# Performance work log

Measured on AMD Instinct MI355X. Metric: run time of the kernel, lower is better.

The kernel has to match this reference:

```python
import jax, jax.numpy as jnp
import numpy as np

N_NODES = 40000
N_EDGES = 640000
D = 128
D_OUT = 128


def _layernorm(x, gamma, beta, eps=1e-5):
    mu = jnp.mean(x, axis=-1, keepdims=True)
    var = jnp.mean(jnp.square(x - mu), axis=-1, keepdims=True)
    return (x - mu) * jax.lax.rsqrt(var + eps) * gamma + beta


def setup_inputs() -> dict:
    key = jax.random.key(0)
    ks = jax.random.split(key, 6)
    x = jax.random.normal(ks[0], (N_NODES, D), dtype=jnp.float32)
    edge_index = jax.random.randint(ks[1], (2, N_EDGES), 0, N_NODES, dtype=jnp.int64)
    s = 1.0 / np.sqrt(D)
    return {
        "x": x,
        "edge_index": edge_index,
        "ln1_w": jnp.ones((D,), jnp.float32),
        "ln1_b": jnp.zeros((D,), jnp.float32),
        "ln2_w": jnp.ones((D,), jnp.float32),
        "ln2_b": jnp.zeros((D,), jnp.float32),
        "w": jnp.ones((D,), jnp.float32),
        "W1": jax.random.normal(ks[2], (D, D), jnp.float32) * s,
        "W2": jax.random.normal(ks[3], (D, D), jnp.float32) * s,
        "O1": jax.random.normal(ks[4], (2 * D, D), jnp.float32) * s,
        "O2": jax.random.normal(ks[5], (D, D_OUT), jnp.float32) * s,
    }


def reference(x, edge_index, ln1_w, ln1_b, ln2_w, ln2_b, w, W1, W2, O1, O2):
    row, col = edge_index[0], edge_index[1]
    n = x.shape[0]
    # gather + 2-layer message MLP (bias-free): [E, D]
    msg = jnp.maximum(x[row] @ W1, 0.0) @ W2
    # scatter_mean over destination nodes (zero where no incoming edges)
    agg = jax.ops.segment_sum(msg, col, num_segments=n)
    cnt = jax.ops.segment_sum(jnp.ones((msg.shape[0],), x.dtype), col, num_segments=n)
    agg = agg / jnp.maximum(cnt, 1.0)[:, None]
    agg_n = _layernorm(agg, ln1_w, ln1_b)
    # repulsion + residual + LayerNorm
    fx = _layernorm(x + (x - agg_n) * w, ln2_w, ln2_b)
    # concat + output MLP
    cat = jnp.concatenate([fx, agg_n], axis=1)
    return jnp.maximum(cat @ O1, 0.0) @ O2
```

## Files before the change

kernel.cpp:

```cpp
#include <hip/hip_runtime.h>
#include <hip/hip_bf16.h>

#define NN 40000
#define NE 640000
#define DD 128
#define CAP 64

typedef __attribute__((ext_vector_type(8))) short bf16x8;
typedef __attribute__((ext_vector_type(8))) unsigned short u16x8;
typedef __attribute__((ext_vector_type(4))) float f32x4;

__device__ __forceinline__ unsigned short f2bf(float f) {
    __hip_bfloat16 h = __float2bfloat16(f);
    return *reinterpret_cast<unsigned short*>(&h);
}
__device__ __forceinline__ float bf2f(unsigned short u) {
    union { unsigned int ui; float f; } v;
    v.ui = ((unsigned int)u) << 16;
    return v.f;
}
__device__ __forceinline__ void gload16(void* lds, const void* g) {
    __builtin_amdgcn_global_load_lds(
        (const __attribute__((address_space(1))) void*)g,
        (__attribute__((address_space(3))) void*)lds, 16, 0, 0);
}

__global__ __launch_bounds__(256) void prep_kernel(
    const float* __restrict__ W1, const float* __restrict__ W2,
    const float* __restrict__ O1, const float* __restrict__ O2,
    unsigned short* __restrict__ w1t, unsigned short* __restrict__ w2t,
    unsigned short* __restrict__ o1t, unsigned short* __restrict__ o2t,
    unsigned int* __restrict__ cnt)
{
    int bx = blockIdx.x;
    if (bx >= 320) {
        int t = (bx - 320) * 256 + threadIdx.x;
        if (t < NN) cnt[t * 16] = 0u;
        return;
    }
    int t = bx * 256 + threadIdx.x;
    if (t < 16384) {
        int n = t >> 7, k = t & 127;
        unsigned b = (unsigned)(n * 256) + (((unsigned)(k * 2)) ^ (((unsigned)(n & 7)) << 4));
        w1t[b >> 1] = f2bf(W1[k * 128 + n]);
    } else if (t < 32768) {
        int i = t - 16384;
        int n = i >> 7, k = i & 127;
        unsigned b = (unsigned)(n * 256) + (((unsigned)(k * 2)) ^ (((unsigned)(n & 7)) << 4));
        w2t[b >> 1] = f2bf(W2[k * 128 + n]);
    } else if (t < 65536) {
        int i = t - 32768;
        int n = i >> 8, k = i & 255;
        unsigned b = (unsigned)(n * 512 + (k >> 7) * 256)
                   + (((unsigned)((k & 127) * 2)) ^ (((unsigned)(n & 7)) << 4));
        o1t[b >> 1] = f2bf(O1[k * 128 + n]);
    } else {
        int i = t - 65536;
        int n = i >> 7, k = i & 127;
        unsigned b = (unsigned)(n * 256) + (((unsigned)(k * 2)) ^ (((unsigned)(n & 7)) << 4));
        o2t[b >> 1] = f2bf(O2[k * 128 + n]);
    }
}

__global__ __launch_bounds__(256) void mlp1_kernel(
    const float* __restrict__ x, const unsigned short* __restrict__ w1t,
    const unsigned short* __restrict__ w2t, unsigned short* __restrict__ nm)
{
    __shared__ unsigned short xt[64 * 128];
    __shared__ unsigned short wb[128 * 128];
    const int tid = threadIdx.x;
    const int row0 = blockIdx.x * 64;
    const int lane = tid & 63;
    const int wv = tid >> 6;

    #pragma unroll
    for (int it = 0; it < 8; ++it) {
        int b = (wv * 8 + it) * 1024;
        gload16((char*)wb + b, (const char*)w1t + b + lane * 16);
    }
    #pragma unroll
    for (int it = 0; it < 4; ++it) {
        int c = tid + it * 256;
        int r = c >> 4;
        int c0 = (c & 15) << 3;
        const float4* gp = reinterpret_cast<const float4*>(x + (size_t)(row0 + r) * DD + c0);
        float4 f0 = gp[0], f1 = gp[1];
        u16x8 p;
        p[0] = f2bf(f0.x); p[1] = f2bf(f0.y); p[2] = f2bf(f0.z); p[3] = f2bf(f0.w);
        p[4] = f2bf(f1.x); p[5] = f2bf(f1.y); p[6] = f2bf(f1.z); p[7] = f2bf(f1.w);
        unsigned b = (unsigned)((r * DD + c0) * 2) ^ ((unsigned)(r & 7) << 4);
        *reinterpret_cast<u16x8*>(reinterpret_cast<char*>(xt) + b) = p;
    }
    __syncthreads();

    const int l15 = lane & 15;
    const int lg = lane >> 4;

    f32x4 acc[8];
    #pragma unroll
    for (int i = 0; i < 8; ++i) acc[i] = (f32x4){0.f, 0.f, 0.f, 0.f};

    #pragma unroll
    for (int kk = 0; kk < 4; ++kk) {
        int k = kk * 32 + lg * 8;
        int ar = wv * 16 + l15;
        bf16x8 a = *reinterpret_cast<const bf16x8*>(
            reinterpret_cast<const char*>(xt) + ((unsigned)((ar * DD + k) * 2) ^ ((unsigned)(ar & 7) << 4)));
        #pragma unroll
        for (int n0 = 0; n0 < 8; ++n0) {
            int bn = n0 * 16 + l15;
            bf16x8 bf = *reinterpret_cast<const bf16x8*>(
                reinterpret_cast<const char*>(wb) + ((unsigned)((bn * DD + k) * 2) ^ ((unsigned)(bn & 7) << 4)));
            acc[n0] = __builtin_amdgcn_mfma_f32_16x16x32_bf16(a, bf, acc[n0], 0, 0, 0);
        }
    }
    __syncthreads();

    #pragma unroll
    for (int it = 0; it < 8; ++it) {
        int b = (wv * 8 + it) * 1024;
        gload16((char*)wb + b, (const char*)w2t + b + lane * 16);
    }
    unsigned short* hb = xt;
    #pragma unroll
    for (int n0 = 0; n0 < 8; ++n0) {
        #pragma unroll
        for (int ri = 0; ri < 4; ++ri) {
            int r = wv * 16 + lg * 4 + ri;
            int cc = n0 * 16 + l15;
            float v = fmaxf(acc[n0][ri], 0.0f);
            *reinterpret_cast<unsigned short*>(
                reinterpret_cast<char*>(hb) + ((unsigned)((r * DD + cc) * 2) ^ ((unsigned)(r & 7) << 4))) = f2bf(v);
        }
    }
    __syncthreads();

    f32x4 acc2[8];
    #pragma unroll
    for (int i = 0; i < 8; ++i) acc2[i] = (f32x4){0.f, 0.f, 0.f, 0.f};
    #pragma unroll
    for (int kk = 0; kk < 4; ++kk) {
        int k = kk * 32 + lg * 8;
        int ar = wv * 16 + l15;
        bf16x8 a = *reinterpret_cast<const bf16x8*>(
            reinterpret_cast<const char*>(hb) + ((unsigned)((ar * DD + k) * 2) ^ ((unsigned)(ar & 7) << 4)));
        #pragma unroll
        for (int n0 = 0; n0 < 8; ++n0) {
            int bn = n0 * 16 + l15;
            bf16x8 bf = *reinterpret_cast<const bf16x8*>(
                reinterpret_cast<const char*>(wb) + ((unsigned)((bn * DD + k) * 2) ^ ((unsigned)(bn & 7) << 4)));
            acc2[n0] = __builtin_amdgcn_mfma_f32_16x16x32_bf16(a, bf, acc2[n0], 0, 0, 0);
        }
    }
    #pragma unroll
    for (int n0 = 0; n0 < 8; ++n0) {
        #pragma unroll
        for (int ri = 0; ri < 4; ++ri) {
            int r = row0 + wv * 16 + lg * 4 + ri;
            int cc = n0 * 16 + l15;
            nm[(size_t)r * DD + cc] = f2bf(acc2[n0][ri]);
        }
    }
}

__global__ __launch_bounds__(256) void fill_kernel(
    const int* __restrict__ ei, unsigned int* __restrict__ cnt,
    unsigned short* __restrict__ srcs)
{
    const int t = blockIdx.x * 256 + threadIdx.x;
    int s[4], d[4];
    #pragma unroll
    for (int j = 0; j < 4; ++j) d[j] = ei[NE + t + j * 160000];
    #pragma unroll
    for (int j = 0; j < 4; ++j) s[j] = ei[t + j * 160000];
    unsigned int p[4];
    #pragma unroll
    for (int j = 0; j < 4; ++j) p[j] = atomicAdd(cnt + d[j] * 16, 1u);
    #pragma unroll
    for (int j = 0; j < 4; ++j)
        if (p[j] < CAP) srcs[(size_t)d[j] * CAP + p[j]] = (unsigned short)s[j];
}

__global__ __launch_bounds__(256) void pull_node_kernel(
    const unsigned short* __restrict__ nm, const unsigned short* __restrict__ srcs,
    const unsigned int* __restrict__ cnt,
    const float* __restrict__ x,
    const float* __restrict__ g1, const float* __restrict__ b1,
    const float* __restrict__ g2, const float* __restrict__ b2,
    const float* __restrict__ w, unsigned short* __restrict__ catb)
{
    const int lane = threadIdx.x & 63;
    const int wv = threadIdx.x >> 6;
    const int i = blockIdx.x * 4 + wv;
    const int d0 = lane * 2;

    const unsigned int degf = cnt[i * 16];
    const int deg = (int)(degf < CAP ? degf : CAP);
    const unsigned short* sp = srcs + (size_t)i * CAP;

    float a0 = 0.f, a1 = 0.f;
    int e = 0;
    for (; e + 8 <= deg; e += 8) {
        int s[8];
        #pragma unroll
        for (int j = 0; j < 8; ++j) s[j] = sp[e + j];
        ushort2 m[8];
        #pragma unroll
        for (int j = 0; j < 8; ++j)
            m[j] = *reinterpret_cast<const ushort2*>(nm + (size_t)s[j] * DD + d0);
        #pragma unroll
        for (int j = 0; j < 8; ++j) { a0 += bf2f(m[j].x); a1 += bf2f(m[j].y); }
    }
    for (; e + 4 <= deg; e += 4) {
        int s0 = sp[e + 0], s1 = sp[e + 1], s2 = sp[e + 2], s3 = sp[e + 3];
        ushort2 m0 = *reinterpret_cast<const ushort2*>(nm + (size_t)s0 * DD + d0);
        ushort2 m1 = *reinterpret_cast<const ushort2*>(nm + (size_t)s1 * DD + d0);
        ushort2 m2 = *reinterpret_cast<const ushort2*>(nm + (size_t)s2 * DD + d0);
        ushort2 m3 = *reinterpret_cast<const ushort2*>(nm + (size_t)s3 * DD + d0);
        a0 += bf2f(m0.x) + bf2f(m1.x) + bf2f(m2.x) + bf2f(m3.x);
        a1 += bf2f(m0.y) + bf2f(m1.y) + bf2f(m2.y) + bf2f(m3.y);
    }
    for (; e < deg; ++e) {
        int s0 = sp[e];
        ushort2 m0 = *reinterpret_cast<const ushort2*>(nm + (size_t)s0 * DD + d0);
        a0 += bf2f(m0.x);
        a1 += bf2f(m0.y);
    }

    float inv = 1.0f / fmaxf((float)degf, 1.0f);
    a0 *= inv; a1 *= inv;

    float s = a0 + a1;
    #pragma unroll
    for (int o = 32; o > 0; o >>= 1) s += __shfl_xor(s, o, 64);
    float mu = s * (1.0f / 128.0f);
    float e0 = a0 - mu, e1 = a1 - mu;
    float q = e0 * e0 + e1 * e1;
    #pragma unroll
    for (int o = 32; o > 0; o >>= 1) q += __shfl_xor(q, o, 64);
    float rs = rsqrtf(q * (1.0f / 128.0f) + 1e-5f);

    float2 g1v = *reinterpret_cast<const float2*>(g1 + d0);
    float2 b1v = *reinterpret_cast<const float2*>(b1 + d0);
    float an0 = e0 * rs * g1v.x + b1v.x;
    float an1 = e1 * rs * g1v.y + b1v.y;

    float2 xv = *reinterpret_cast<const float2*>(x + (size_t)i * DD + d0);
    float2 wv2 = *reinterpret_cast<const float2*>(w + d0);
    float t0 = xv.x + (xv.x - an0) * wv2.x;
    float t1 = xv.y + (xv.y - an1) * wv2.y;

    float s2 = t0 + t1;
    #pragma unroll
    for (int o = 32; o > 0; o >>= 1) s2 += __shfl_xor(s2, o, 64);
    float mu2 = s2 * (1.0f / 128.0f);
    float f0 = t0 - mu2, f1 = t1 - mu2;
    float q2 = f0 * f0 + f1 * f1;
    #pragma unroll
    for (int o = 32; o > 0; o >>= 1) q2 += __shfl_xor(q2, o, 64);
    float rs2 = rsqrtf(q2 * (1.0f / 128.0f) + 1e-5f);

    float2 g2v = *reinterpret_cast<const float2*>(g2 + d0);
    float2 b2v = *reinterpret_cast<const float2*>(b2 + d0);
    float fx0 = f0 * rs2 * g2v.x + b2v.x;
    float fx1 = f1 * rs2 * g2v.y + b2v.y;

    ushort2 uo; uo.x = f2bf(fx0); uo.y = f2bf(fx1);
    *reinterpret_cast<ushort2*>(catb + (size_t)i * 256 + d0) = uo;
    ushort2 ua; ua.x = f2bf(an0); ua.y = f2bf(an1);
    *reinterpret_cast<ushort2*>(catb + (size_t)i * 256 + 128 + d0) = ua;
}

__global__ __launch_bounds__(256) void mlp2_kernel(
    const unsigned short* __restrict__ catb, const unsigned short* __restrict__ o1t,
    const unsigned short* __restrict__ o2t, float* __restrict__ out)
{
    __shared__ unsigned short ct[64 * 128];
    __shared__ unsigned short wb[128 * 128];
    const int tid = threadIdx.x;
    const int row0 = blockIdx.x * 64;
    const int lane = tid & 63;
    const int wv = tid >> 6;
    const int l15 = lane & 15;
    const int lg = lane >> 4;

    f32x4 acc[8];
    #pragma unroll
    for (int i = 0; i < 8; ++i) acc[i] = (f32x4){0.f, 0.f, 0.f, 0.f};

    for (int h = 0; h < 2; ++h) {
        #pragma unroll
        for (int it = 0; it < 8; ++it) {
            int Lb = (wv * 8 + it) * 1024;
            int n = (Lb >> 8) + (lane >> 4);
            int c2 = (lane & 15) * 16;
            gload16((char*)wb + Lb, (const char*)o1t + n * 512 + h * 256 + c2);
        }
        #pragma unroll
        for (int it = 0; it < 4; ++it) {
            int c = tid + it * 256;
            int r = c >> 4;
            int c0 = (c & 15) << 3;
            u16x8 v = *reinterpret_cast<const u16x8*>(catb + (size_t)(row0 + r) * 256 + h * 128 + c0);
            unsigned b = (unsigned)((r * 128 + c0) * 2) ^ ((unsigned)(r & 7) << 4);
            *reinterpret_cast<u16x8*>(reinterpret_cast<char*>(ct) + b) = v;
        }
        __syncthreads();
        #pragma unroll
        for (int kk = 0; kk < 4; ++kk) {
            int k = kk * 32 + lg * 8;
            int ar = wv * 16 + l15;
            bf16x8 a = *reinterpret_cast<const bf16x8*>(
                reinterpret_cast<const char*>(ct) + ((unsigned)((ar * 128 + k) * 2) ^ ((unsigned)(ar & 7) << 4)));
            #pragma unroll
            for (int n0 = 0; n0 < 8; ++n0) {
                int bn = n0 * 16 + l15;
                bf16x8 bf = *reinterpret_cast<const bf16x8*>(
                    reinterpret_cast<const char*>(wb) + ((unsigned)((bn * 128 + k) * 2) ^ ((unsigned)(bn & 7) << 4)));
                acc[n0] = __builtin_amdgcn_mfma_f32_16x16x32_bf16(a, bf, acc[n0], 0, 0, 0);
            }
        }
        __syncthreads();
    }

    #pragma unroll
    for (int it = 0; it < 8; ++it) {
        int b = (wv * 8 + it) * 1024;
        gload16((char*)wb + b, (const char*)o2t + b + lane * 16);
    }
    unsigned short* hb = ct;
    #pragma unroll
    for (int n0 = 0; n0 < 8; ++n0) {
        #pragma unroll
        for (int ri = 0; ri < 4; ++ri) {
            int r = wv * 16 + lg * 4 + ri;
            int cc = n0 * 16 + l15;
            float v = fmaxf(acc[n0][ri], 0.0f);
            *reinterpret_cast<unsigned short*>(
                reinterpret_cast<char*>(hb) + ((unsigned)((r * DD + cc) * 2) ^ ((unsigned)(r & 7) << 4))) = f2bf(v);
        }
    }
    __syncthreads();

    f32x4 acc2[8];
    #pragma unroll
    for (int i = 0; i < 8; ++i) acc2[i] = (f32x4){0.f, 0.f, 0.f, 0.f};
    #pragma unroll
    for (int kk = 0; kk < 4; ++kk) {
        int k = kk * 32 + lg * 8;
        int ar = wv * 16 + l15;
        bf16x8 a = *reinterpret_cast<const bf16x8*>(
            reinterpret_cast<const char*>(hb) + ((unsigned)((ar * DD + k) * 2) ^ ((unsigned)(ar & 7) << 4)));
        #pragma unroll
        for (int n0 = 0; n0 < 8; ++n0) {
            int bn = n0 * 16 + l15;
            bf16x8 bf = *reinterpret_cast<const bf16x8*>(
                reinterpret_cast<const char*>(wb) + ((unsigned)((bn * DD + k) * 2) ^ ((unsigned)(bn & 7) << 4)));
            acc2[n0] = __builtin_amdgcn_mfma_f32_16x16x32_bf16(a, bf, acc2[n0], 0, 0, 0);
        }
    }

    #pragma unroll
    for (int n0 = 0; n0 < 8; ++n0) {
        #pragma unroll
        for (int ri = 0; ri < 4; ++ri) {
            int r = row0 + wv * 16 + lg * 4 + ri;
            int cc = n0 * 16 + l15;
            out[(size_t)r * DD + cc] = acc2[n0][ri];
        }
    }
}

extern "C" void kernel_launch(void* const* d_in, const int* in_sizes, int n_in,
                              void* d_out, int out_size, void* d_ws, size_t ws_size,
                              hipStream_t stream) {
    const float* x   = (const float*)d_in[0];
    const int*   ei  = (const int*)d_in[1];
    const float* g1  = (const float*)d_in[2];
    const float* b1  = (const float*)d_in[3];
    const float* g2  = (const float*)d_in[4];
    const float* b2  = (const float*)d_in[5];
    const float* w   = (const float*)d_in[6];
    const float* W1  = (const float*)d_in[7];
    const float* W2  = (const float*)d_in[8];
    const float* O1  = (const float*)d_in[9];
    const float* O2  = (const float*)d_in[10];
    float* out = (float*)d_out;

    char* ws = (char*)d_ws;
    unsigned short* nm   = (unsigned short*)(ws);
    unsigned short* catb = (unsigned short*)(ws + 10240000);
    unsigned short* srcs = (unsigned short*)(ws + 30720000);
    unsigned int*   cnt  = (unsigned int*)(ws + 35840000);
    unsigned short* w1t  = (unsigned short*)(ws + 38400000);
    unsigned short* w2t  = (unsigned short*)(ws + 38432768);
    unsigned short* o1t  = (unsigned short*)(ws + 38465536);
    unsigned short* o2t  = (unsigned short*)(ws + 38531072);

    prep_kernel<<<477, 256, 0, stream>>>(W1, W2, O1, O2, w1t, w2t, o1t, o2t, cnt);
    fill_kernel<<<625, 256, 0, stream>>>(ei, cnt, srcs);
    mlp1_kernel<<<625, 256, 0, stream>>>(x, w1t, w2t, nm);
    pull_node_kernel<<<NN / 4, 256, 0, stream>>>(nm, srcs, cnt, x, g1, b1, g2, b2, w, catb);
    mlp2_kernel<<<NN / 64, 256, 0, stream>>>(catb, o1t, o2t, out);
}
```

Measured before the change: 170.1 us.

## Fuse neighbor pull and layernorms into output MLP kernel via LDS

Merges the per-node aggregation and layernorm kernel with the output MLP into one 512-thread kernel. Each block gathers 64 nodes, writes the concatenated bf16 features straight into shared memory, then runs both output matmuls with 8 waves splitting the N dimension. This removes the global round-trip of the concat buffer and one launch. The cost is only 625 blocks with 48KB+ LDS each, which lowers occupancy and leaves the latency-bound gather phase with less overlap.

Result: slower. 197.8 us (+16.3%).

```diff
diff --git a/kernel.cpp b/kernel.cpp
--- a/kernel.cpp
+++ b/kernel.cpp
@@ -62,6 +62,24 @@
     }
 }
 
+__global__ __launch_bounds__(256) void fill_kernel(
+    const int* __restrict__ ei, unsigned int* __restrict__ cnt,
+    unsigned short* __restrict__ srcs)
+{
+    const int t = blockIdx.x * 256 + threadIdx.x;
+    int s[4], d[4];
+    #pragma unroll
+    for (int j = 0; j < 4; ++j) d[j] = ei[NE + t + j * 160000];
+    #pragma unroll
+    for (int j = 0; j < 4; ++j) s[j] = ei[t + j * 160000];
+    unsigned int p[4];
+    #pragma unroll
+    for (int j = 0; j < 4; ++j) p[j] = atomicAdd(cnt + d[j] * 16, 1u);
+    #pragma unroll
+    for (int j = 0; j < 4; ++j)
+        if (p[j] < CAP) srcs[(size_t)d[j] * CAP + p[j]] = (unsigned short)s[j];
+}
+
 __global__ __launch_bounds__(256) void mlp1_kernel(
     const float* __restrict__ x, const unsigned short* __restrict__ w1t,
     const unsigned short* __restrict__ w2t, unsigned short* __restrict__ nm)
@@ -163,178 +181,167 @@
     }
 }
 
-__global__ __launch_bounds__(256) void fill_kernel(
-    const int* __restrict__ ei, unsigned int* __restrict__ cnt,
-    unsigned short* __restrict__ srcs)
-{
-    const int t = blockIdx.x * 256 + threadIdx.x;
-    int s[4], d[4];
-    #pragma unroll
-    for (int j = 0; j < 4; ++j) d[j] = ei[NE + t + j * 160000];
-    #pragma unroll
-    for (int j = 0; j < 4; ++j) s[j] = ei[t + j * 160000];
-    unsigned int p[4];
-    #pragma unroll
-    for (int j = 0; j < 4; ++j) p[j] = atomicAdd(cnt + d[j] * 16, 1u);
-    #pragma unroll
-    for (int j = 0; j < 4; ++j)
-        if (p[j] < CAP) srcs[(size_t)d[j] * CAP + p[j]] = (unsigned short)s[j];
-}
-
-__global__ __launch_bounds__(256) void pull_node_kernel(
+__global__ __launch_bounds__(512) void mega2_kernel(
     const unsigned short* __restrict__ nm, const unsigned short* __restrict__ srcs,
     const unsigned int* __restrict__ cnt,
     const float* __restrict__ x,
     const float* __restrict__ g1, const float* __restrict__ b1,
     const float* __restrict__ g2, const float* __restrict__ b2,
-    const float* __restrict__ w, unsigned short* __restrict__ catb)
+    const float* __restrict__ w,
+    const unsigned short* __restrict__ o1t, const unsigned short* __restrict__ o2t,
+    float* __restrict__ out)
 {
-    const int lane = threadIdx.x & 63;
-    const int wv = threadIdx.x >> 6;
-    const int i = blockIdx.x * 4 + wv;
-    const int d0 = lane * 2;
-
-    const unsigned int degf = cnt[i * 16];
-    const int deg = (int)(degf < CAP ? degf : CAP);
-    const unsigned short* sp = srcs + (size_t)i * CAP;
-
-    float a0 = 0.f, a1 = 0.f;
-    int e = 0;
-    for (; e + 8 <= deg; e += 8) {
-        int s[8];
-        #pragma unroll
-        for (int j = 0; j < 8; ++j) s[j] = sp[e + j];
-        ushort2 m[8];
-        #pragma unroll
-        for (int j = 0; j < 8; ++j)
-            m[j] = *reinterpret_cast<const ushort2*>(nm + (size_t)s[j] * DD + d0);
-        #pragma unroll
-        for (int j = 0; j < 8; ++j) { a0 += bf2f(m[j].x); a1 += bf2f(m[j].y); }
-    }
-    for (; e + 4 <= deg; e += 4) {
-        int s0 = sp[e + 0], s1 = sp[e + 1], s2 = sp[e + 2], s3 = sp[e + 3];
-        ushort2 m0 = *reinterpret_cast<const ushort2*>(nm + (size_t)s0 * DD + d0);
-        ushort2 m1 = *reinterpret_cast<const ushort2*>(nm + (size_t)s1 * DD + d0);
-        ushort2 m2 = *reinterpret_cast<const ushort2*>(nm + (size_t)s2 * DD + d0);
-        ushort2 m3 = *reinterpret_cast<const ushort2*>(nm + (size_t)s3 * DD + d0);
-        a0 += bf2f(m0.x) + bf2f(m1.x) + bf2f(m2.x) + bf2f(m3.x);
-        a1 += bf2f(m0.y) + bf2f(m1.y) + bf2f(m2.y) + bf2f(m3.y);
-    }
-    for (; e < deg; ++e) {
-        int s0 = sp[e];
-        ushort2 m0 = *reinterpret_cast<const ushort2*>(nm + (size_t)s0 * DD + d0);
-        a0 += bf2f(m0.x);
-        a1 += bf2f(m0.y);
-    }
-
-    float inv = 1.0f / fmaxf((float)degf, 1.0f);
-    a0 *= inv; a1 *= inv;
-
-    float s = a0 + a1;
-    #pragma unroll
-    for (int o = 32; o > 0; o >>= 1) s += __shfl_xor(s, o, 64);
-    float mu = s * (1.0f / 128.0f);
-    float e0 = a0 - mu, e1 = a1 - mu;
-    float q = e0 * e0 + e1 * e1;
-    #pragma unroll
-    for (int o = 32; o > 0; o >>= 1) q += __shfl_xor(q, o, 64);
-    float rs = rsqrtf(q * (1.0f / 128.0f) + 1e-5f);
-
-    float2 g1v = *reinterpret_cast<const float2*>(g1 + d0);
-    float2 b1v = *reinterpret_cast<const float2*>(b1 + d0);
-    float an0 = e0 * rs * g1v.x + b1v.x;
-    float an1 = e1 * rs * g1v.y + b1v.y;
-
-    float2 xv = *reinterpret_cast<const float2*>(x + (size_t)i * DD + d0);
-    float2 wv2 = *reinterpret_cast<const float2*>(w + d0);
-    float t0 = xv.x + (xv.x - an0) * wv2.x;
-    float t1 = xv.y + (xv.y - an1) * wv2.y;
-
-    float s2 = t0 + t1;
-    #pragma unroll
-    for (int o = 32; o > 0; o >>= 1) s2 += __shfl_xor(s2, o, 64);
-    float mu2 = s2 * (1.0f / 128.0f);
-    float f0 = t0 - mu2, f1 = t1 - mu2;
-    float q2 = f0 * f0 + f1 * f1;
-    #pragma unroll
-    for (int o = 32; o > 0; o >>= 1) q2 += __shfl_xor(q2, o, 64);
-    float rs2 = rsqrtf(q2 * (1.0f / 128.0f) + 1e-5f);
-
-    float2 g2v = *reinterpret_cast<const float2*>(g2 + d0);
-    float2 b2v = *reinterpret_cast<const float2*>(b2 + d0);
-    float fx0 = f0 * rs2 * g2v.x + b2v.x;
-    float fx1 = f1 * rs2 * g2v.y + b2v.y;
-
-    ushort2 uo; uo.x = f2bf(fx0); uo.y = f2bf(fx1);
-    *reinterpret_cast<ushort2*>(catb + (size_t)i * 256 + d0) = uo;
-    ushort2 ua; ua.x = f2bf(an0); ua.y = f2bf(an1);
-    *reinterpret_cast<ushort2*>(catb + (size_t)i * 256 + 128 + d0) = ua;
-}
-
-__global__ __launch_bounds__(256) void mlp2_kernel(
-    const unsigned short* __restrict__ catb, const unsigned short* __restrict__ o1t,
-    const unsigned short* __restrict__ o2t, float* __restrict__ out)
-{
-    __shared__ unsigned short ct[64 * 128];
+    __shared__ unsigned short ct[64 * 256];
     __shared__ unsigned short wb[128 * 128];
     const int tid = threadIdx.x;
     const int row0 = blockIdx.x * 64;
     const int lane = tid & 63;
     const int wv = tid >> 6;
+
+    #pragma unroll
+    for (int it = 0; it < 4; ++it) {
+        int Lb = (wv * 4 + it) * 1024;
+        int n = (Lb >> 8) + (lane >> 4);
+        int c2 = (lane & 15) * 16;
+        gload16((char*)wb + Lb, (const char*)o1t + n * 512 + 0 * 256 + c2);
+    }
+
+    const int d0 = lane * 2;
+    for (int t = 0; t < 8; ++t) {
+        const int i = row0 + wv + 8 * t;
+        const int r = wv + 8 * t;
+
+        const unsigned int degf = cnt[i * 16];
+        const int deg = (int)(degf < CAP ? degf : CAP);
+        const unsigned short* sp = srcs + (size_t)i * CAP;
+
+        float a0 = 0.f, a1 = 0.f;
+        int e = 0;
+        for (; e + 8 <= deg; e += 8) {
+            int s[8];
+            #pragma unroll
+            for (int j = 0; j < 8; ++j) s[j] = sp[e + j];
+            ushort2 m[8];
+            #pragma unroll
+            for (int j = 0; j < 8; ++j)
+                m[j] = *reinterpret_cast<const ushort2*>(nm + (size_t)s[j] * DD + d0);
+            #pragma unroll
+            for (int j = 0; j < 8; ++j) { a0 += bf2f(m[j].x); a1 += bf2f(m[j].y); }
+        }
+        for (; e + 4 <= deg; e += 4) {
+            int s0 = sp[e + 0], s1 = sp[e + 1], s2 = sp[e + 2], s3 = sp[e + 3];
+            ushort2 m0 = *reinterpret_cast<const ushort2*>(nm + (size_t)s0 * DD + d0);
+            ushort2 m1 = *reinterpret_cast<const ushort2*>(nm + (size_t)s1 * DD + d0);
+            ushort2 m2 = *reinterpret_cast<const ushort2*>(nm + (size_t)s2 * DD + d0);
+            ushort2 m3 = *reinterpret_cast<const ushort2*>(nm + (size_t)s3 * DD + d0);
+            a0 += bf2f(m0.x) + bf2f(m1.x) + bf2f(m2.x) + bf2f(m3.x);
+            a1 += bf2f(m0.y) + bf2f(m1.y) + bf2f(m2.y) + bf2f(m3.y);
+        }
+        for (; e < deg; ++e) {
+            int s0 = sp[e];
+            ushort2 m0 = *reinterpret_cast<const ushort2*>(nm + (size_t)s0 * DD + d0);
+            a0 += bf2f(m0.x);
+            a1 += bf2f(m0.y);
+        }
+
+        float inv = 1.0f / fmaxf((float)degf, 1.0f);
+        a0 *= inv; a1 *= inv;
+
+        float s = a0 + a1;
+        #pragma unroll
+        for (int o = 32; o > 0; o >>= 1) s += __shfl_xor(s, o, 64);
+        float mu = s * (1.0f / 128.0f);
+        float e0 = a0 - mu, e1 = a1 - mu;
+        float q = e0 * e0 + e1 * e1;
+        #pragma unroll
+        for (int o = 32; o > 0; o >>= 1) q += __shfl_xor(q, o, 64);
+        float rs = rsqrtf(q * (1.0f / 128.0f) + 1e-5f);
+
+        float2 g1v = *reinterpret_cast<const float2*>(g1 + d0);
+        float2 b1v = *reinterpret_cast<const float2*>(b1 + d0);
+        float an0 = e0 * rs * g1v.x + b1v.x;
+        float an1 = e1 * rs * g1v.y + b1v.y;
+
+        float2 xv = *reinterpret_cast<const float2*>(x + (size_t)i * DD + d0);
+        float2 wv2 = *reinterpret_cast<const float2*>(w + d0);
+        float t0 = xv.x + (xv.x - an0) * wv2.x;
+        float t1 = xv.y + (xv.y - an1) * wv2.y;
+
+        float s2 = t0 + t1;
+        #pragma unroll
+        for (int o = 32; o > 0; o >>= 1) s2 += __shfl_xor(s2, o, 64);
+        float mu2 = s2 * (1.0f / 128.0f);
+        float f0 = t0 - mu2, f1 = t1 - mu2;
+        float q2 = f0 * f0 + f1 * f1;
+        #pragma unroll
+        for (int o = 32; o > 0; o >>= 1) q2 += __shfl_xor(q2, o, 64);
+        float rs2 = rsqrtf(q2 * (1.0f / 128.0f) + 1e-5f);
+
+        float2 g2v = *reinterpret_cast<const float2*>(g2 + d0);
+        float2 b2v = *reinterpret_cast<const float2*>(b2 + d0);
+        float fx0 = f0 * rs2 * g2v.x + b2v.x;
+        float fx1 = f1 * rs2 * g2v.y + b2v.y;
+
+        ushort2 uo; uo.x = f2bf(fx0); uo.y = f2bf(fx1);
+        *reinterpret_cast<ushort2*>(reinterpret_cast<char*>(ct) +
+            ((unsigned)((r * 256 + d0) * 2) ^ ((unsigned)(r & 7) << 4))) = uo;
+        ushort2 ua; ua.x = f2bf(an0); ua.y = f2bf(an1);
+        *reinterpret_cast<ushort2*>(reinterpret_cast<char*>(ct) +
+            ((unsigned)((r * 256 + 128 + d0) * 2) ^ ((unsigned)(r & 7) << 4))) = ua;
+    }
+    __syncthreads();
+
     const int l15 = lane & 15;
     const int lg = lane >> 4;
-
-    f32x4 acc[8];
-    #pragma unroll
-    for (int i = 0; i < 8; ++i) acc[i] = (f32x4){0.f, 0.f, 0.f, 0.f};
+    const int wr = wv & 3;
+    const int nh = wv >> 2;
+
+    f32x4 acc[4];
+    #pragma unroll
+    for (int i = 0; i < 4; ++i) acc[i] = (f32x4){0.f, 0.f, 0.f, 0.f};
 
     for (int h = 0; h < 2; ++h) {
-        #pragma unroll
-        for (int it = 0; it < 8; ++it) {
-            int Lb = (wv * 8 + it) * 1024;
-            int n = (Lb >> 8) + (lane >> 4);
-            int c2 = (lane & 15) * 16;
-            gload16((char*)wb + Lb, (const char*)o1t + n * 512 + h * 256 + c2);
-        }
-        #pragma unroll
-        for (int it = 0; it < 4; ++it) {
-            int c = tid + it * 256;
-            int r = c >> 4;
-            int c0 = (c & 15) << 3;
-            u16x8 v = *reinterpret_cast<const u16x8*>(catb + (size_t)(row0 + r) * 256 + h * 128 + c0);
-            unsigned b = (unsigned)((r * 128 + c0) * 2) ^ ((unsigned)(r & 7) << 4);
-            *reinterpret_cast<u16x8*>(reinterpret_cast<char*>(ct) + b) = v;
-        }
-        __syncthreads();
+        if (h == 1) {
+            __syncthreads();
+            #pragma unroll
+            for (int it = 0; it < 4; ++it) {
+                int Lb = (wv * 4 + it) * 1024;
+                int n = (Lb >> 8) + (lane >> 4);
+                int c2 = (lane & 15) * 16;
+                gload16((char*)wb + Lb, (const char*)o1t + n * 512 + 256 + c2);
+            }
+            __syncthreads();
+        }
         #pragma unroll
         for (int kk = 0; kk < 4; ++kk) {
             int k = kk * 32 + lg * 8;
-            int ar = wv * 16 + l15;
+            int ar = wr * 16 + l15;
             bf16x8 a = *reinterpret_cast<const bf16x8*>(
-                reinterpret_cast<const char*>(ct) + ((unsigned)((ar * 128 + k) * 2) ^ ((unsigned)(ar & 7) << 4)));
+                reinterpret_cast<const char*>(ct) +
+                ((unsigned)((ar * 256 + h * 128 + k) * 2) ^ ((unsigned)(ar & 7) << 4)));
             #pragma unroll
-            for (int n0 = 0; n0 < 8; ++n0) {
-                int bn = n0 * 16 + l15;
+            for (int n0 = 0; n0 < 4; ++n0) {
+                int bn = (nh * 4 + n0) * 16 + l15;
                 bf16x8 bf = *reinterpret_cast<const bf16x8*>(
                     reinterpret_cast<const char*>(wb) + ((unsigned)((bn * 128 + k) * 2) ^ ((unsigned)(bn & 7) << 4)));
                 acc[n0] = __builtin_amdgcn_mfma_f32_16x16x32_bf16(a, bf, acc[n0], 0, 0, 0);
             }
         }
-        __syncthreads();
-    }
-
-    #pragma unroll
-    for (int it = 0; it < 8; ++it) {
-        int b = (wv * 8 + it) * 1024;
+    }
+    __syncthreads();
+
+    #pragma unroll
+    for (int it = 0; it < 4; ++it) {
+        int b = (wv * 4 + it) * 1024;
         gload16((char*)wb + b, (const char*)o2t + b + lane * 16);
     }
     unsigned short* hb = ct;
     #pragma unroll
-    for (int n0 = 0; n0 < 8; ++n0) {
+    for (int n0 = 0; n0 < 4; ++n0) {
         #pragma unroll
         for (int ri = 0; ri < 4; ++ri) {
-            int r = wv * 16 + lg * 4 + ri;
-            int cc = n0 * 16 + l15;
+            int r = wr * 16 + lg * 4 + ri;
+            int cc = (nh * 4 + n0) * 16 + l15;
             float v = fmaxf(acc[n0][ri], 0.0f);
             *reinterpret_cast<unsigned short*>(
                 reinterpret_cast<char*>(hb) + ((unsigned)((r * DD + cc) * 2) ^ ((unsigned)(r & 7) << 4))) = f2bf(v);
@@ -342,18 +349,18 @@
     }
     __syncthreads();
 
-    f32x4 acc2[8];
-    #pragma unroll
-    for (int i = 0; i < 8; ++i) acc2[i] = (f32x4){0.f, 0.f, 0.f, 0.f};
+    f32x4 acc2[4];
+    #pragma unroll
+    for (int i = 0; i < 4; ++i) acc2[i] = (f32x4){0.f, 0.f, 0.f, 0.f};
     #pragma unroll
     for (int kk = 0; kk < 4; ++kk) {
         int k = kk * 32 + lg * 8;
-        int ar = wv * 16 + l15;
+        int ar = wr * 16 + l15;
         bf16x8 a = *reinterpret_cast<const bf16x8*>(
             reinterpret_cast<const char*>(hb) + ((unsigned)((ar * DD + k) * 2) ^ ((unsigned)(ar & 7) << 4)));
         #pragma unroll
-        for (int n0 = 0; n0 < 8; ++n0) {
-            int bn = n0 * 16 + l15;
+        for (int n0 = 0; n0 < 4; ++n0) {
+            int bn = (nh * 4 + n0) * 16 + l15;
             bf16x8 bf = *reinterpret_cast<const bf16x8*>(
                 reinterpret_cast<const char*>(wb) + ((unsigned)((bn * DD + k) * 2) ^ ((unsigned)(bn & 7) << 4)));
             acc2[n0] = __builtin_amdgcn_mfma_f32_16x16x32_bf16(a, bf, acc2[n0], 0, 0, 0);
@@ -361,11 +368,11 @@
     }
 
     #pragma unroll
-    for (int n0 = 0; n0 < 8; ++n0) {
+    for (int n0 = 0; n0 < 4; ++n0) {
         #pragma unroll
         for (int ri = 0; ri < 4; ++ri) {
-            int r = row0 + wv * 16 + lg * 4 + ri;
-            int cc = n0 * 16 + l15;
+            int r = row0 + wr * 16 + lg * 4 + ri;
+            int cc = (nh * 4 + n0) * 16 + l15;
             out[(size_t)r * DD + cc] = acc2[n0][ri];
         }
     }
@@ -389,17 +396,15 @@
 
     char* ws = (char*)d_ws;
     unsigned short* nm   = (unsigned short*)(ws);
-    unsigned short* catb = (unsigned short*)(ws + 10240000);
-    unsigned short* srcs = (unsigned short*)(ws + 30720000);
-    unsigned int*   cnt  = (unsigned int*)(ws + 35840000);
-    unsigned short* w1t  = (unsigned short*)(ws + 38400000);
-    unsigned short* w2t  = (unsigned short*)(ws + 38432768);
-    unsigned short* o1t  = (unsigned short*)(ws + 38465536);
-    unsigned short* o2t  = (unsigned short*)(ws + 38531072);
+    unsigned short* srcs = (unsigned short*)(ws + 10240000);
+    unsigned int*   cnt  = (unsigned int*)(ws + 15360000);
+    unsigned short* w1t  = (unsigned short*)(ws + 17920000);
+    unsigned short* w2t  = (unsigned short*)(ws + 17952768);
+    unsigned short* o1t  = (unsigned short*)(ws + 17985536);
+    unsigned short* o2t  = (unsigned short*)(ws + 18051072);
 
     prep_kernel<<<477, 256, 0, stream>>>(W1, W2, O1, O2, w1t, w2t, o1t, o2t, cnt);
     fill_kernel<<<625, 256, 0, stream>>>(ei, cnt, srcs);
     mlp1_kernel<<<625, 256, 0, stream>>>(x, w1t, w2t, nm);
-    pull_node_kernel<<<NN / 4, 256, 0, stream>>>(nm, srcs, cnt, x, g1, b1, g2, b2, w, catb);
-    mlp2_kernel<<<NN / 64, 256, 0, stream>>>(catb, o1t, o2t, out);
-}
+    mega2_kernel<<<625, 512, 0, stream>>>(nm, srcs, cnt, x, g1, b1, g2, b2, w, o1t, o2t, out);
+}
```
